# Performance work log

Hardware: AMD Instinct MI355X
Metric: run time of the kernel (lower is better)

## Reference

```python
import jax, jax.numpy as jnp
import numpy as np

BATCH = 2097152
HIDDEN = 64
N_BINS = 8
TAIL_BOUND = 5.0
FIX_DIM = 0


def setup_inputs() -> dict:
    key = jax.random.key(0)
    ks = jax.random.split(key, 7)
    s = 0.05  # small-init style scaling to keep spline params well-conditioned
    return {
        "x": jax.random.normal(ks[0], (BATCH, 2), dtype=jnp.float32),
        "W1": jax.random.normal(ks[1], (HIDDEN, 1), dtype=jnp.float32) * s,
        "b1": jax.random.normal(ks[2], (HIDDEN,), dtype=jnp.float32) * s,
        "W2": jax.random.normal(ks[3], (HIDDEN, HIDDEN), dtype=jnp.float32) * s,
        "b2": jax.random.normal(ks[4], (HIDDEN,), dtype=jnp.float32) * s,
        "W3": jax.random.normal(ks[5], (3 * N_BINS + 1, HIDDEN), dtype=jnp.float32) * s,
        "b3": jax.random.normal(ks[6], (3 * N_BINS + 1,), dtype=jnp.float32) * s,
    }


def _rqs_forward(inputs, widths, heights, derivs, tail_bound):
    # inputs: (B,); widths/heights: (B, K); derivs: (B, K+1)
    K = widths.shape[-1]
    inside = (inputs >= -tail_bound) & (inputs <= tail_bound)
    w = jax.nn.softmax(widths, axis=-1) * (2 * tail_bound)
    h = jax.nn.softmax(heights, axis=-1) * (2 * tail_bound)
    d = jax.nn.softplus(derivs) + 0.001
    cw = jnp.pad(jnp.cumsum(w, axis=-1), ((0, 0), (1, 0))) - tail_bound  # (B, K+1)
    ch = jnp.pad(jnp.cumsum(h, axis=-1), ((0, 0), (1, 0))) - tail_bound
    # torch.searchsorted(cw[:,1:], v) with right=False == count of knots strictly < v
    bin_idx = jnp.sum(cw[:, 1:] < inputs[:, None], axis=-1)
    bin_idx = jnp.clip(bin_idx, 0, K - 1)

    def take(a, i):
        return jnp.take_along_axis(a, i[:, None], axis=-1)[:, 0]

    w_k = take(w, bin_idx)
    h_k = take(h, bin_idx)
    x_k = take(cw, bin_idx)
    y_k = take(ch, bin_idx)
    d_k = take(d, bin_idx)
    d_k1 = take(d, bin_idx + 1)
    s_k = h_k / w_k
    xi = jnp.clip((inputs - x_k) / w_k, 0.0, 1.0)
    one_m = 1.0 - xi
    denom = s_k + (d_k1 + d_k - 2.0 * s_k) * xi * one_m
    outputs = y_k + h_k * (s_k * xi * xi + d_k * xi * one_m) / denom
    numer = s_k * s_k * (d_k1 * xi * xi + 2.0 * s_k * xi * one_m + d_k * one_m * one_m)
    log_det = jnp.log(numer) - 2.0 * jnp.log(denom)
    outputs = jnp.where(inside, outputs, inputs)
    log_det = jnp.where(inside, log_det, jnp.zeros_like(log_det))
    return outputs, log_det


def reference(x, W1, b1, W2, b2, W3, b3):
    x_fix = x[:, FIX_DIM:FIX_DIM + 1]        # (B, 1)
    x_var = x[:, 1 - FIX_DIM]                # (B,)
    h = jax.nn.relu(x_fix @ W1.T + b1)       # (B, H)
    h = jax.nn.relu(h @ W2.T + b2)           # (B, H)
    raw = h @ W3.T + b3                      # (B, 3K+1)
    Wp = raw[:, :N_BINS]
    Hp = raw[:, N_BINS:2 * N_BINS]
    Dp = raw[:, 2 * N_BINS:]
    y_var, log_det = _rqs_forward(x_var, Wp, Hp, Dp, TAIL_BOUND)
    if FIX_DIM == 0:
        y = jnp.concatenate([x_fix, y_var[:, None]], axis=1)
    else:
        y = jnp.concatenate([y_var[:, None], x_fix], axis=1)
    return y, log_det
```

## Files before the change

### kernel.cpp

```cpp
#include <hip/hip_runtime.h>
#include <hip/hip_fp16.h>
#include <math.h>

#define NB 8
#define TB 5.0f
#define HID 64
#define XLO -8.0f
#define XHI 8.0f
#define TT 512


__device__ inline unsigned pk(float a, float b) {
    return (unsigned)__half_as_ushort(__float2half(a))
         | ((unsigned)__half_as_ushort(__float2half(b)) << 16);
}
__device__ inline void dec2(unsigned u, float& a, float& b) {
    __half2 h = *reinterpret_cast<const __half2*>(&u);
    float2 f = __half22float2(h);
    a = f.x; b = f.y;
}

__global__ __launch_bounds__(512) void build_table_kernel(
    const float* __restrict__ W1, const float* __restrict__ b1,
    const float* __restrict__ W2, const float* __restrict__ b2,
    const float* __restrict__ W3, const float* __restrict__ b3,
    uint4* __restrict__ table, int T)
{
    __shared__ float part_raw[8][64][25];
    int lt = threadIdx.x;
    int lane = lt & 63;
    int part = __builtin_amdgcn_readfirstlane(lt >> 6);
    int node = blockIdx.x * 64 + lane;
    int nodec = min(node, T);
    float xf = XLO + (XHI - XLO) * ((float)nodec / (float)T);

    float h1[HID];
#pragma unroll
    for (int k = 0; k < HID; ++k)
        h1[k] = fmaxf(fmaf(xf, W1[k], b1[k]), 0.f);

    float r[25];
#pragma unroll
    for (int m = 0; m < 25; ++m) r[m] = 0.f;

    int j0 = part * 8;
#pragma unroll
    for (int jj = 0; jj < 8; ++jj) {
        int j = j0 + jj;
        float a0 = b2[j], a1 = 0.f, a2 = 0.f, a3 = 0.f;
#pragma unroll
        for (int k = 0; k < HID; k += 4) {
            a0 = fmaf(h1[k+0], W2[j*HID + k+0], a0);
            a1 = fmaf(h1[k+1], W2[j*HID + k+1], a1);
            a2 = fmaf(h1[k+2], W2[j*HID + k+2], a2);
            a3 = fmaf(h1[k+3], W2[j*HID + k+3], a3);
        }
        float h2 = fmaxf((a0 + a1) + (a2 + a3), 0.f);
#pragma unroll
        for (int m = 0; m < 25; ++m)
            r[m] = fmaf(h2, W3[m*HID + j], r[m]);
    }
#pragma unroll
    for (int m = 0; m < 25; ++m) part_raw[part][lane][m] = r[m];
    __syncthreads();

    if (part == 0 && node <= T) {
        float raw[25];
#pragma unroll
        for (int m = 0; m < 25; ++m) {
            float s01 = part_raw[0][lane][m] + part_raw[1][lane][m];
            float s23 = part_raw[2][lane][m] + part_raw[3][lane][m];
            float s45 = part_raw[4][lane][m] + part_raw[5][lane][m];
            float s67 = part_raw[6][lane][m] + part_raw[7][lane][m];
            raw[m] = b3[m] + ((s01 + s23) + (s45 + s67));
        }

        float w[NB], h[NB], dd[NB + 1];
        {
            float mw = raw[0];
#pragma unroll
            for (int k = 1; k < NB; ++k) mw = fmaxf(mw, raw[k]);
            float s = 0.f;
#pragma unroll
            for (int k = 0; k < NB; ++k) { w[k] = __expf(raw[k] - mw); s += w[k]; }
            float inv = (2.f * TB) / s;
#pragma unroll
            for (int k = 0; k < NB; ++k) w[k] *= inv;
        }
        {
            float mh = raw[NB];
#pragma unroll
            for (int k = 1; k < NB; ++k) mh = fmaxf(mh, raw[NB + k]);
            float s = 0.f;
#pragma unroll
            for (int k = 0; k < NB; ++k) { h[k] = __expf(raw[NB + k] - mh); s += h[k]; }
            float inv = (2.f * TB) / s;
#pragma unroll
            for (int k = 0; k < NB; ++k) h[k] *= inv;
        }
#pragma unroll
        for (int k = 0; k < NB + 1; ++k) {
            float v = raw[2 * NB + k];
            dd[k] = fmaxf(v, 0.f) + log1pf(__expf(-fabsf(v))) + 0.001f;
        }

        float e[24];
        float cw = -TB, ch = -TB;
#pragma unroll
        for (int k = 0; k < 7; ++k) { cw += w[k]; e[k] = cw; }
#pragma unroll
        for (int k = 0; k < 7; ++k) { ch += h[k]; e[7 + k] = ch; }
#pragma unroll
        for (int k = 0; k < 9; ++k) e[14 + k] = dd[k];
        e[23] = 0.f;

        uint4* dst = table + (size_t)node * 3;
        dst[0] = make_uint4(pk(e[0],e[1]),  pk(e[2],e[3]),  pk(e[4],e[5]),   pk(e[6],e[7]));
        dst[1] = make_uint4(pk(e[8],e[9]),  pk(e[10],e[11]),pk(e[12],e[13]), pk(e[14],e[15]));
        dst[2] = make_uint4(pk(e[16],e[17]),pk(e[18],e[19]),pk(e[20],e[21]), pk(e[22],e[23]));
    }
}

#define TAB_U4 ((TT + 1) * 3)

__global__ __launch_bounds__(256) void spline_eval_kernel(
    const float* __restrict__ x,
    const uint4* __restrict__ table,
    float* __restrict__ out,
    int n, float inv_dx)
{
    __shared__ uint4 tab[TAB_U4];
    for (int idx = threadIdx.x; idx < TAB_U4; idx += 256)
        tab[idx] = table[idx];
    __syncthreads();

    int i = blockIdx.x * blockDim.x + threadIdx.x;
    if (i >= n) return;

    float2 xv2 = ((const float2*)x)[i];
    float xf = xv2.x;
    float xv = xv2.y;

    int c = (int)((xf - XLO) * inv_dx + 0.5f);
    c = min(max(c, 0), TT);
    int base = c * 3;
    uint4 q0 = tab[base], q1 = tab[base + 1], q2 = tab[base + 2];

    float e[24];
    dec2(q0.x, e[0],  e[1]);  dec2(q0.y, e[2],  e[3]);
    dec2(q0.z, e[4],  e[5]);  dec2(q0.w, e[6],  e[7]);
    dec2(q1.x, e[8],  e[9]);  dec2(q1.y, e[10], e[11]);
    dec2(q1.z, e[12], e[13]); dec2(q1.w, e[14], e[15]);
    dec2(q2.x, e[16], e[17]); dec2(q2.y, e[18], e[19]);
    dec2(q2.z, e[20], e[21]); dec2(q2.w, e[22], e[23]);

    float cw[9], ch[9], d[9];
    cw[0] = -TB; ch[0] = -TB; cw[8] = TB; ch[8] = TB;
#pragma unroll
    for (int k = 1; k < 8; ++k) { cw[k] = e[k - 1]; ch[k] = e[6 + k]; }
#pragma unroll
    for (int k = 0; k < 9; ++k) d[k] = e[14 + k];

    float xk = cw[0], yk = ch[0];
    float wk = cw[1] - cw[0], hk = ch[1] - ch[0];
    float dk = d[0], dk1 = d[1];
#pragma unroll
    for (int kk = 1; kk < 8; ++kk) {
        bool take = cw[kk] < xv;
        xk  = take ? cw[kk]            : xk;
        yk  = take ? ch[kk]            : yk;
        wk  = take ? cw[kk+1] - cw[kk] : wk;
        hk  = take ? ch[kk+1] - ch[kk] : hk;
        dk  = take ? d[kk]             : dk;
        dk1 = take ? d[kk+1]           : dk1;
    }

    float rw = __builtin_amdgcn_rcpf(wk);
    float sk = hk * rw;
    float t  = (xv - xk) * rw;
    t = fminf(fmaxf(t, 0.f), 1.f);
    float om = 1.f - t;
    float denom = sk + (dk1 + dk - 2.f * sk) * t * om;
    float rd = __builtin_amdgcn_rcpf(denom);
    float outp  = yk + hk * (sk * t * t + dk * t * om) * rd;
    float numer = sk * sk * (dk1 * t * t + 2.f * sk * t * om + dk * om * om);
    float ld = __logf(numer * rd * rd);

    bool inside = (xv >= -TB) && (xv <= TB);
    float yv = inside ? outp : xv;
    ld = inside ? ld : 0.f;

    ((float2*)out)[i] = make_float2(xf, yv);
    out[2 * n + i] = ld;
}

extern "C" void kernel_launch(void* const* d_in, const int* in_sizes, int n_in,
                              void* d_out, int out_size, void* d_ws, size_t ws_size,
                              hipStream_t stream) {
    const float* x  = (const float*)d_in[0];
    const float* W1 = (const float*)d_in[1];
    const float* b1 = (const float*)d_in[2];
    const float* W2 = (const float*)d_in[3];
    const float* b2 = (const float*)d_in[4];
    const float* W3 = (const float*)d_in[5];
    const float* b3 = (const float*)d_in[6];
    float* out   = (float*)d_out;
    uint4* table = (uint4*)d_ws;

    int n = in_sizes[0] / 2;
    float inv_dx = (float)TT / (XHI - XLO);

    int nodes = TT + 1;
    build_table_kernel<<<(nodes + 63) / 64, 512, 0, stream>>>(
        W1, b1, W2, b2, W3, b3, table, TT);
    spline_eval_kernel<<<(n + 255) / 256, 256, 0, stream>>>(
        x, table, out, n, inv_dx);
}
```

Baseline: 111.0 us.

## Process two samples per thread and read spline table from global cache

The eval kernel stops staging the whole 24.6KB table into LDS in every block and instead reads each sample's three table rows straight from global memory, relying on L1/L2 caching. Each thread now handles two samples, with float4 loads of x, float4 stores of y and float2 stores of log-det. The aim is to remove the per-block table copy and barrier and to widen memory transactions. In exchange, table lookups become scattered global gathers instead of LDS reads, and an odd n would drop its last element.

```diff
diff --git a/kernel.cpp b/kernel.cpp
--- a/kernel.cpp
+++ b/kernel.cpp
@@ -8,7 +8,6 @@
 #define XLO -8.0f
 #define XHI 8.0f
 #define TT 512
-
 
 __device__ inline unsigned pk(float a, float b) {
     return (unsigned)__half_as_ushort(__float2half(a))
@@ -121,31 +120,9 @@
     }
 }
 
-#define TAB_U4 ((TT + 1) * 3)
-
-__global__ __launch_bounds__(256) void spline_eval_kernel(
-    const float* __restrict__ x,
-    const uint4* __restrict__ table,
-    float* __restrict__ out,
-    int n, float inv_dx)
+__device__ inline void rqs_one(float xv, uint4 q0, uint4 q1, uint4 q2,
+                               float& yv, float& ld)
 {
-    __shared__ uint4 tab[TAB_U4];
-    for (int idx = threadIdx.x; idx < TAB_U4; idx += 256)
-        tab[idx] = table[idx];
-    __syncthreads();
-
-    int i = blockIdx.x * blockDim.x + threadIdx.x;
-    if (i >= n) return;
-
-    float2 xv2 = ((const float2*)x)[i];
-    float xf = xv2.x;
-    float xv = xv2.y;
-
-    int c = (int)((xf - XLO) * inv_dx + 0.5f);
-    c = min(max(c, 0), TT);
-    int base = c * 3;
-    uint4 q0 = tab[base], q1 = tab[base + 1], q2 = tab[base + 2];
-
     float e[24];
     dec2(q0.x, e[0],  e[1]);  dec2(q0.y, e[2],  e[3]);
     dec2(q0.z, e[4],  e[5]);  dec2(q0.w, e[6],  e[7]);
@@ -184,14 +161,40 @@
     float rd = __builtin_amdgcn_rcpf(denom);
     float outp  = yk + hk * (sk * t * t + dk * t * om) * rd;
     float numer = sk * sk * (dk1 * t * t + 2.f * sk * t * om + dk * om * om);
-    float ld = __logf(numer * rd * rd);
+    float l = __logf(numer * rd * rd);
 
     bool inside = (xv >= -TB) && (xv <= TB);
-    float yv = inside ? outp : xv;
-    ld = inside ? ld : 0.f;
-
-    ((float2*)out)[i] = make_float2(xf, yv);
-    out[2 * n + i] = ld;
+    yv = inside ? outp : xv;
+    ld = inside ? l : 0.f;
+}
+
+__global__ __launch_bounds__(256) void spline_eval_kernel(
+    const float4* __restrict__ x4,
+    const uint4* __restrict__ table,
+    float4* __restrict__ outy,
+    float2* __restrict__ outld,
+    int half_n, float inv_dx)
+{
+    int i = blockIdx.x * blockDim.x + threadIdx.x;
+    if (i >= half_n) return;
+
+    float4 xx = x4[i];
+
+    int cA = (int)fmaf(xx.x - XLO, inv_dx, 0.5f);
+    int cB = (int)fmaf(xx.z - XLO, inv_dx, 0.5f);
+    cA = min(max(cA, 0), TT);
+    cB = min(max(cB, 0), TT);
+    const uint4* rA = table + cA * 3;
+    const uint4* rB = table + cB * 3;
+    uint4 a0 = rA[0], a1 = rA[1], a2 = rA[2];
+    uint4 b0 = rB[0], b1 = rB[1], b2 = rB[2];
+
+    float yA, ldA, yB, ldB;
+    rqs_one(xx.y, a0, a1, a2, yA, ldA);
+    rqs_one(xx.w, b0, b1, b2, yB, ldB);
+
+    outy[i]  = make_float4(xx.x, yA, xx.z, yB);
+    outld[i] = make_float2(ldA, ldB);
 }
 
 extern "C" void kernel_launch(void* const* d_in, const int* in_sizes, int n_in,
@@ -213,6 +216,9 @@
     int nodes = TT + 1;
     build_table_kernel<<<(nodes + 63) / 64, 512, 0, stream>>>(
         W1, b1, W2, b2, W3, b3, table, TT);
-    spline_eval_kernel<<<(n + 255) / 256, 256, 0, stream>>>(
-        x, table, out, n, inv_dx);
-}
+
+    int half_n = n / 2;
+    spline_eval_kernel<<<(half_n + 255) / 256, 256, 0, stream>>>(
+        (const float4*)x, table, (float4*)out, (float2*)(out + 2 * (size_t)n),
+        half_n, inv_dx);
+}
```

Result: faster. 107.6 us (-3.0%).
